# Kernel tuning notes

Hardware: AMD Instinct MI355X
Metric: run time of the kernel (lower is better)

The kernel has to match this reference:

```python
import jax, jax.numpy as jnp
import numpy as np

# J1 Bessel function of the first kind, single-precision rational/asymptotic
# approximation (Numerical Recipes / Abramowitz & Stegun 9.4), matching
# scipy.special.j1 to ~1e-7 relative accuracy. Fully on-device, jit-able.

def bessel_j1(x):
    ax = jnp.abs(x)
    small = ax < 8.0

    # |x| < 8: rational approximation in y = x^2
    y = x * x
    num = x * (72362614232.0 + y * (-7895059235.0 + y * (242396853.1
          + y * (-2972611.439 + y * (15704.48260 + y * (-30.16036606))))))
    den = 144725228442.0 + y * (2300535178.0 + y * (18583304.74
          + y * (99447.43394 + y * (376.9991397 + y))))
    small_val = num / den

    # |x| >= 8: asymptotic expansion; guard ax to avoid div-by-zero in the
    # untaken branch under jnp.where
    ax_s = jnp.where(small, 8.0, ax)
    z = 8.0 / ax_s
    yy = z * z
    xx = ax_s - 2.356194491  # ax - 3*pi/4
    p1 = 1.0 + yy * (0.183105e-2 + yy * (-0.3516396496e-4
         + yy * (0.2457520174e-5 + yy * (-0.240337019e-6))))
    p2 = 0.04687499995 + yy * (-0.2002690873e-3 + yy * (0.8449199096e-5
         + yy * (-0.88228987e-6 + yy * 0.105787412e-6)))
    big_val = jnp.sqrt(0.636619772 / ax_s) * (jnp.cos(xx) * p1
              - z * jnp.sin(xx) * p2) * jnp.sign(x)

    return jnp.where(small, small_val, big_val)


def setup_inputs() -> dict:
    key = jax.random.key(0)
    ks = jax.random.split(key, 7)
    B, D_in, H, D_out = 32768, 64, 2048, 64
    s1 = 1.0 / np.sqrt(D_in)
    s2 = 1.0 / np.sqrt(H)
    return {
        "t": jax.random.normal(ks[0], (B, D_in), dtype=jnp.float32),
        "W1": jax.random.normal(ks[1], (D_in, H), dtype=jnp.float32) * s1,
        "b1": jax.random.normal(ks[2], (H,), dtype=jnp.float32) * s1,
        "W2": jax.random.normal(ks[3], (H, H), dtype=jnp.float32) * s2,
        "b2": jax.random.normal(ks[4], (H,), dtype=jnp.float32) * s2,
        "W3": jax.random.normal(ks[5], (H, D_out), dtype=jnp.float32) * s2,
        "b3": jax.random.normal(ks[6], (D_out,), dtype=jnp.float32) * s2,
    }


def reference(t, W1, b1, W2, b2, W3, b3):
    h = bessel_j1(t @ W1 + b1)        # Linear -> J1 Bessel
    h = jnp.sin(h @ W2 + b2)          # Linear -> sin
    return h @ W3 + b3                # Linear
```

## Files before the change

### kernel.cpp

```cpp
#include <hip/hip_runtime.h>
#include <cstdint>
#include <cstddef>

typedef unsigned short u16;
typedef __attribute__((ext_vector_type(8))) __bf16 bf16x8;
typedef __attribute__((ext_vector_type(4))) float f32x4;


__device__ __forceinline__ u16 f2bf(float f) {
    union { float f; unsigned u; } v; v.f = f;
    unsigned r = v.u + 0x7fffu + ((v.u >> 16) & 1u);
    return (u16)(r >> 16);
}

__device__ __forceinline__ float j1f_approx(float x) {
    float ax = fabsf(x);
    float y = x * x;
    float num = x * (7.2362614232e10f + y * (-7.895059235e9f + y * (2.423968531e8f
              + y * (-2.972611439e6f + y * (1.570448260e4f + y * (-3.016036606e1f))))));
    float den = 1.44725228442e11f + y * (2.300535178e9f + y * (1.858330474e7f
              + y * (9.944743394e4f + y * (3.769991397e2f + y))));
    float r = num / den;
    if (__any(ax >= 8.0f)) {
        float z  = 8.0f / ax;
        float yy = z * z;
        float xx = ax - 2.356194491f;
        float p1 = 1.0f + yy * (0.183105e-2f + yy * (-0.3516396496e-4f
                 + yy * (0.2457520174e-5f + yy * (-0.240337019e-6f))));
        float p2 = 0.04687499995f + yy * (-0.2002690873e-3f + yy * (0.8449199096e-5f
                 + yy * (-0.88228987e-6f + yy * 0.105787412e-6f)));
        float big = sqrtf(0.636619772f / ax) * (__cosf(xx) * p1 - z * __sinf(xx) * p2);
        big = copysignf(big, x);
        if (ax >= 8.0f) r = big;
    }
    return r;
}


__global__ void k_f32_to_bf16(const float* __restrict__ in, u16* __restrict__ out, int n) {
    int i = blockIdx.x * 256 + threadIdx.x;
    if (i < n) out[i] = f2bf(in[i]);
}

__global__ void k_transpose_bf16(const float* __restrict__ in, u16* __restrict__ out,
                                 int K, int N) {
    __shared__ float tile[32][33];
    int n0 = blockIdx.x * 32, k0 = blockIdx.y * 32;
    int tx = threadIdx.x, ty = threadIdx.y;
    #pragma unroll
    for (int i = ty; i < 32; i += 8)
        tile[i][tx] = in[(size_t)(k0 + i) * N + n0 + tx];
    __syncthreads();
    #pragma unroll
    for (int i = ty; i < 32; i += 8)
        out[(size_t)(n0 + i) * K + k0 + tx] = f2bf(tile[tx][i]);
}

__global__ void k_init_out(const float* __restrict__ b3, float* __restrict__ out, int n) {
    int i = blockIdx.x * 256 + threadIdx.x;
    if (i < n) out[i] = b3[i & 63];
}


#define BK 32

template<int BM, int BN, int WTM, int WTN, int EPI>
__global__ __launch_bounds__(256)
void k_gemm_bt(const u16* __restrict__ A, int lda,
               const u16* __restrict__ Bt, int ldb,
               const float* __restrict__ bias,
               void* __restrict__ Cout, int ldc,
               int kstart, int klen)
{
    __shared__ __align__(16) u16 Alds[BM * BK];
    __shared__ __align__(16) u16 Blds[BN * BK];

    const int tid  = threadIdx.x;
    const int lane = tid & 63;
    const int wid  = tid >> 6;
    const int wrow = (wid >> 1) * (WTM * 16);
    const int wcol = (wid & 1) * (WTN * 16);
    const int lr   = lane & 15;
    const int lkb  = (lane >> 4) * 8;

    const int brow = blockIdx.y * BM;
    const int bcol = blockIdx.x * BN;
    const int k0 = kstart + blockIdx.z * klen;
    const int k1 = k0 + klen;

    f32x4 acc[WTM][WTN] = {};

    for (int kk = k0; kk < k1; kk += BK) {
        #pragma unroll
        for (int c = tid; c < BM * 4; c += 256) {
            const u16* g = A + (size_t)(brow + (c >> 2)) * lda + kk + (c & 3) * 8;
            __builtin_amdgcn_global_load_lds(
                (const __attribute__((address_space(1))) void*)g,
                (__attribute__((address_space(3))) void*)(&Alds[c * 8]), 16, 0, 0);
        }
        #pragma unroll
        for (int c = tid; c < BN * 4; c += 256) {
            const u16* g = Bt + (size_t)(bcol + (c >> 2)) * ldb + kk + (c & 3) * 8;
            __builtin_amdgcn_global_load_lds(
                (const __attribute__((address_space(1))) void*)g,
                (__attribute__((address_space(3))) void*)(&Blds[c * 8]), 16, 0, 0);
        }
        __syncthreads();

        bf16x8 af[WTM], bfr[WTN];
        #pragma unroll
        for (int m = 0; m < WTM; ++m)
            af[m] = *(const bf16x8*)&Alds[(wrow + m * 16 + lr) * BK + lkb];
        #pragma unroll
        for (int n = 0; n < WTN; ++n)
            bfr[n] = *(const bf16x8*)&Blds[(wcol + n * 16 + lr) * BK + lkb];
        #pragma unroll
        for (int m = 0; m < WTM; ++m)
            #pragma unroll
            for (int n = 0; n < WTN; ++n)
                acc[m][n] = __builtin_amdgcn_mfma_f32_16x16x32_bf16(
                                af[m], bfr[n], acc[m][n], 0, 0, 0);
        __syncthreads();
    }

    const int rbase = brow + wrow + (lane >> 4) * 4;
    const int cbase = bcol + wcol + lr;
    #pragma unroll
    for (int n = 0; n < WTN; ++n) {
        const int col = cbase + n * 16;
        float bv = 0.0f;
        if constexpr (EPI != 2) bv = bias[col];
        #pragma unroll
        for (int m = 0; m < WTM; ++m) {
            #pragma unroll
            for (int r = 0; r < 4; ++r) {
                const int row = rbase + m * 16 + r;
                float v = acc[m][n][r];
                if constexpr (EPI == 0) {
                    ((u16*)Cout)[(size_t)row * ldc + col] = f2bf(j1f_approx(v + bv));
                } else {
                    atomicAdd(&((float*)Cout)[(size_t)row * ldc + col], v);
                }
            }
        }
    }
}


__global__ __launch_bounds__(512, 2)
void k_gemm256(const u16* __restrict__ A, int lda,
               const u16* __restrict__ Bt, int ldb,
               const float* __restrict__ bias,
               u16* __restrict__ C, int ldc, int K)
{
    __shared__ __align__(16) u16 lds[65536];

    const int tid  = threadIdx.x;
    const int lane = tid & 63;
    const int wid  = tid >> 6;
    const int wr   = wid >> 2;
    const int wc   = wid & 3;
    const int lr   = lane & 15;
    const int kq   = lane >> 4;

    const int nwg  = gridDim.x * gridDim.y;
    const int bid0 = blockIdx.y * gridDim.x + blockIdx.x;
    const int wg   = (bid0 & 7) * (nwg >> 3) + (bid0 >> 3);
    const int bx   = wg % gridDim.x;
    const int by   = wg / gridDim.x;
    const int brow = by * 256;
    const int bcol = bx * 256;

    const int nT = K >> 6;

    auto stage = [&](int tile, int q) {
        const int b = tile & 1, h = q & 1;
        const u16* gb; int ldg; u16* lb;
        if (q < 2) { gb = A  + (size_t)(brow + h * 128) * lda; ldg = lda;
                     lb = &lds[b * 16384 + h * 8192]; }
        else       { gb = Bt + (size_t)(bcol + h * 128) * ldb; ldg = ldb;
                     lb = &lds[32768 + b * 16384 + h * 8192]; }
        #pragma unroll
        for (int r = 0; r < 2; ++r) {
            const int c = r * 512 + tid;
            const int row = c >> 3, slot = c & 7;
            const u16* g = gb + (size_t)row * ldg + tile * 64 + ((slot ^ (row & 7)) << 3);
            __builtin_amdgcn_global_load_lds(
                (const __attribute__((address_space(1))) void*)g,
                (__attribute__((address_space(3))) void*)(lb + c * 8), 16, 0, 0);
        }
    };

    int a_off[8][2], b_off[4][2];
    #pragma unroll
    for (int m = 0; m < 8; ++m) {
        const int row = m * 16 + lr;
        #pragma unroll
        for (int ks = 0; ks < 2; ++ks)
            a_off[m][ks] = row * 64 + ((ks * 32 + kq * 8) ^ ((row & 7) << 3));
    }
    #pragma unroll
    for (int n = 0; n < 4; ++n) {
        const int row = (wc & 1) * 64 + n * 16 + lr;
        #pragma unroll
        for (int ks = 0; ks < 2; ++ks)
            b_off[n][ks] = row * 64 + ((ks * 32 + kq * 8) ^ ((row & 7) << 3));
    }

    f32x4 acc[8][4] = {};
    bf16x8 af[4][2], bf[2][2];

#define RD_A(mh) { _Pragma("unroll") for (int m = 0; m < 4; ++m) \
                   _Pragma("unroll") for (int ks = 0; ks < 2; ++ks) \
                       af[m][ks] = *(const bf16x8*)&la[a_off[(mh)*4 + m][ks]]; }
#define RD_B(nh) { _Pragma("unroll") for (int j = 0; j < 2; ++j) \
                   _Pragma("unroll") for (int ks = 0; ks < 2; ++ks) \
                       bf[j][ks] = *(const bf16x8*)&lb_[b_off[(nh)*2 + j][ks]]; }
#define MMA(mh, nh) { __builtin_amdgcn_s_setprio(1); \
                      _Pragma("unroll") for (int m = 0; m < 4; ++m) \
                      _Pragma("unroll") for (int j = 0; j < 2; ++j) \
                      _Pragma("unroll") for (int ks = 0; ks < 2; ++ks) \
                          acc[(mh)*4 + m][(nh)*2 + j] = \
                              __builtin_amdgcn_mfma_f32_16x16x32_bf16( \
                                  af[m][ks], bf[j][ks], acc[(mh)*4 + m][(nh)*2 + j], 0, 0, 0); \
                      __builtin_amdgcn_s_setprio(0); }
#define BARRIER()  asm volatile("s_barrier" ::: "memory")
#define LGKM0()    asm volatile("s_waitcnt lgkmcnt(0)" ::: "memory")

    stage(0, 0); stage(0, 1); stage(0, 2); stage(0, 3);
    if (nT > 1) {
        stage(1, 0); stage(1, 1);
        asm volatile("s_waitcnt vmcnt(4)" ::: "memory");
    } else {
        asm volatile("s_waitcnt vmcnt(0)" ::: "memory");
    }
    BARRIER();

    for (int t = 0; t < nT; ++t) {
        const int b = t & 1;
        const u16* la  = &lds[b * 16384 + wr * 8192];
        const u16* lb_ = &lds[32768 + b * 16384 + (wc >> 1) * 8192];

        RD_A(0); RD_B(0);
        if (t + 1 < nT) stage(t + 1, 2);
        BARRIER(); LGKM0();
        MMA(0, 0);
        BARRIER();

        RD_B(1);
        if (t + 1 < nT) stage(t + 1, 3);
        BARRIER(); LGKM0();
        MMA(0, 1);
        BARRIER();

        RD_A(1);
        BARRIER(); LGKM0();
        MMA(1, 1);
        BARRIER();

        RD_B(0);
        if (t + 2 < nT) { stage(t + 2, 0); stage(t + 2, 1); }
        BARRIER(); LGKM0();
        MMA(1, 0);
        if (t < nT - 2)       { asm volatile("s_waitcnt vmcnt(4)" ::: "memory"); }
        else if (t == nT - 2) { asm volatile("s_waitcnt vmcnt(0)" ::: "memory"); }
        BARRIER();
    }

#undef RD_A
#undef RD_B
#undef MMA
#undef BARRIER
#undef LGKM0

    #pragma unroll
    for (int n = 0; n < 4; ++n) {
        const int col = bcol + wc * 64 + n * 16 + lr;
        const float bv = bias[col];
        #pragma unroll
        for (int m = 0; m < 8; ++m) {
            const int row = brow + wr * 128 + m * 16 + kq * 4;
            #pragma unroll
            for (int r = 0; r < 4; ++r)
                C[(size_t)(row + r) * ldc + col] = f2bf(__sinf(acc[m][n][r] + bv));
        }
    }
}


extern "C" void kernel_launch(void* const* d_in, const int* in_sizes, int n_in,
                              void* d_out, int out_size, void* d_ws, size_t ws_size,
                              hipStream_t stream) {
    const float* t  = (const float*)d_in[0];
    const float* W1 = (const float*)d_in[1];
    const float* b1 = (const float*)d_in[2];
    const float* W2 = (const float*)d_in[3];
    const float* b2 = (const float*)d_in[4];
    const float* W3 = (const float*)d_in[5];
    const float* b3 = (const float*)d_in[6];
    float* out = (float*)d_out;

    constexpr int B = 32768, Din = 64, H = 2048, Dout = 64;

    char* p = (char*)d_ws;
    u16* t_bf = (u16*)p; p += (size_t)B * Din * 2;
    u16* w1t  = (u16*)p; p += (size_t)H * Din * 2;
    u16* w2t  = (u16*)p; p += (size_t)H * H * 2;
    u16* w3t  = (u16*)p; p += (size_t)Dout * H * 2;
    size_t fixed = (size_t)(p - (char*)d_ws);

    int R = B;
    while (R > 512 && fixed + (size_t)2 * R * H * 2 > ws_size) R >>= 1;
    u16* h1 = (u16*)p;
    u16* h2 = (u16*)(p + (size_t)R * H * 2);

    k_f32_to_bf16<<<(B * Din + 255) / 256, 256, 0, stream>>>(t, t_bf, B * Din);
    k_transpose_bf16<<<dim3(H / 32, Din / 32), dim3(32, 8), 0, stream>>>(W1, w1t, Din, H);
    k_transpose_bf16<<<dim3(H / 32, H / 32), dim3(32, 8), 0, stream>>>(W2, w2t, H, H);
    k_transpose_bf16<<<dim3(Dout / 32, H / 32), dim3(32, 8), 0, stream>>>(W3, w3t, H, Dout);
    k_init_out<<<(out_size + 255) / 256, 256, 0, stream>>>(b3, out, out_size);

    const int SPLITS = 4;
    for (int c0 = 0; c0 < B; c0 += R) {
        const u16* tA = t_bf + (size_t)c0 * Din;
        k_gemm_bt<128, 128, 4, 4, 0><<<dim3(H / 128, R / 128), 256, 0, stream>>>(
            tA, Din, w1t, Din, b1, h1, H, 0, Din);
        k_gemm256<<<dim3(H / 256, R / 256), 512, 0, stream>>>(
            h1, H, w2t, H, b2, h2, H, H);
        k_gemm_bt<128, 64, 4, 2, 2><<<dim3(1, R / 128, SPLITS), 256, 0, stream>>>(
            h2, H, w3t, H, nullptr, out + (size_t)c0 * Dout, Dout, 0, H / SPLITS);
    }
}
```

Before: 410.4 us.

## Restructure big GEMM main loop to overlap LDS fragment reads with MFMA

Reworks the 256x256 GEMM main loop so the B-fragment LDS reads and the second A-fragment read are issued right after the preceding MFMA batch instead of before a barrier plus lgkmcnt(0) wait. Two B fragment register sets are used so the reads can overlap the matrix math, and sched_barrier hints keep the compiler from reordering across phases. Global staging addresses are precomputed once per thread rather than recomputed in a lambda, and the epilogue loads bias values up front. The explicit lgkmcnt waits are removed, which relies on compiler-inserted waits for correctness, and the extra fragment registers raise register pressure.

```diff
diff --git a/kernel.cpp b/kernel.cpp
--- a/kernel.cpp
+++ b/kernel.cpp
@@ -5,6 +5,9 @@
 typedef unsigned short u16;
 typedef __attribute__((ext_vector_type(8))) __bf16 bf16x8;
 typedef __attribute__((ext_vector_type(4))) float f32x4;
+
+#define AS1(p) ((const __attribute__((address_space(1))) void*)(p))
+#define AS3(p) ((__attribute__((address_space(3))) void*)(p))
 
 
 __device__ __forceinline__ u16 f2bf(float f) {
@@ -94,16 +97,12 @@
         #pragma unroll
         for (int c = tid; c < BM * 4; c += 256) {
             const u16* g = A + (size_t)(brow + (c >> 2)) * lda + kk + (c & 3) * 8;
-            __builtin_amdgcn_global_load_lds(
-                (const __attribute__((address_space(1))) void*)g,
-                (__attribute__((address_space(3))) void*)(&Alds[c * 8]), 16, 0, 0);
+            __builtin_amdgcn_global_load_lds(AS1(g), AS3(&Alds[c * 8]), 16, 0, 0);
         }
         #pragma unroll
         for (int c = tid; c < BN * 4; c += 256) {
             const u16* g = Bt + (size_t)(bcol + (c >> 2)) * ldb + kk + (c & 3) * 8;
-            __builtin_amdgcn_global_load_lds(
-                (const __attribute__((address_space(1))) void*)g,
-                (__attribute__((address_space(3))) void*)(&Blds[c * 8]), 16, 0, 0);
+            __builtin_amdgcn_global_load_lds(AS1(g), AS3(&Blds[c * 8]), 16, 0, 0);
         }
         __syncthreads();
 
@@ -173,22 +172,18 @@
 
     const int nT = K >> 6;
 
-    auto stage = [&](int tile, int q) {
-        const int b = tile & 1, h = q & 1;
-        const u16* gb; int ldg; u16* lb;
-        if (q < 2) { gb = A  + (size_t)(brow + h * 128) * lda; ldg = lda;
-                     lb = &lds[b * 16384 + h * 8192]; }
-        else       { gb = Bt + (size_t)(bcol + h * 128) * ldb; ldg = ldb;
-                     lb = &lds[32768 + b * 16384 + h * 8192]; }
-        #pragma unroll
-        for (int r = 0; r < 2; ++r) {
-            const int c = r * 512 + tid;
-            const int row = c >> 3, slot = c & 7;
-            const u16* g = gb + (size_t)row * ldg + tile * 64 + ((slot ^ (row & 7)) << 3);
-            __builtin_amdgcn_global_load_lds(
-                (const __attribute__((address_space(1))) void*)g,
-                (__attribute__((address_space(3))) void*)(lb + c * 8), 16, 0, 0);
-        }
+    const int srow = tid >> 3;
+    const int swz  = (((tid & 7) ^ (srow & 7)) << 3);
+    const u16* pgA0 = A  + (size_t)(brow +       srow) * lda + swz;
+    const u16* pgA1 = A  + (size_t)(brow + 128 + srow) * lda + swz;
+    const u16* pgB0 = Bt + (size_t)(bcol +       srow) * ldb + swz;
+    const u16* pgB1 = Bt + (size_t)(bcol + 128 + srow) * ldb + swz;
+
+    auto stg = [&](const u16* base, int ldg, int tile, u16* l0) {
+        __builtin_amdgcn_global_load_lds(AS1(base + tile * 64),
+                                         AS3(l0 + tid * 8), 16, 0, 0);
+        __builtin_amdgcn_global_load_lds(AS1(base + (size_t)64 * ldg + tile * 64),
+                                         AS3(l0 + 4096 + tid * 8), 16, 0, 0);
     };
 
     int a_off[8][2], b_off[4][2];
@@ -208,28 +203,35 @@
     }
 
     f32x4 acc[8][4] = {};
-    bf16x8 af[4][2], bf[2][2];
+    bf16x8 af[4][2], bf0[2][2], bf1[2][2];
 
 #define RD_A(mh) { _Pragma("unroll") for (int m = 0; m < 4; ++m) \
                    _Pragma("unroll") for (int ks = 0; ks < 2; ++ks) \
                        af[m][ks] = *(const bf16x8*)&la[a_off[(mh)*4 + m][ks]]; }
-#define RD_B(nh) { _Pragma("unroll") for (int j = 0; j < 2; ++j) \
+#define RD_B0()  { _Pragma("unroll") for (int j = 0; j < 2; ++j) \
                    _Pragma("unroll") for (int ks = 0; ks < 2; ++ks) \
-                       bf[j][ks] = *(const bf16x8*)&lb_[b_off[(nh)*2 + j][ks]]; }
-#define MMA(mh, nh) { __builtin_amdgcn_s_setprio(1); \
+                       bf0[j][ks] = *(const bf16x8*)&lb_[b_off[j][ks]]; }
+#define RD_B1()  { _Pragma("unroll") for (int j = 0; j < 2; ++j) \
+                   _Pragma("unroll") for (int ks = 0; ks < 2; ++ks) \
+                       bf1[j][ks] = *(const bf16x8*)&lb_[b_off[2 + j][ks]]; }
+#define MMA(mh, nh, BF) { __builtin_amdgcn_s_setprio(1); \
                       _Pragma("unroll") for (int m = 0; m < 4; ++m) \
                       _Pragma("unroll") for (int j = 0; j < 2; ++j) \
                       _Pragma("unroll") for (int ks = 0; ks < 2; ++ks) \
                           acc[(mh)*4 + m][(nh)*2 + j] = \
                               __builtin_amdgcn_mfma_f32_16x16x32_bf16( \
-                                  af[m][ks], bf[j][ks], acc[(mh)*4 + m][(nh)*2 + j], 0, 0, 0); \
+                                  af[m][ks], BF[j][ks], acc[(mh)*4 + m][(nh)*2 + j], 0, 0, 0); \
                       __builtin_amdgcn_s_setprio(0); }
 #define BARRIER()  asm volatile("s_barrier" ::: "memory")
-#define LGKM0()    asm volatile("s_waitcnt lgkmcnt(0)" ::: "memory")
-
-    stage(0, 0); stage(0, 1); stage(0, 2); stage(0, 3);
+#define SCHED0()   __builtin_amdgcn_sched_barrier(0)
+
+    stg(pgA0, lda, 0, &lds[0]);
+    stg(pgA1, lda, 0, &lds[8192]);
+    stg(pgB0, ldb, 0, &lds[32768]);
+    stg(pgB1, ldb, 0, &lds[32768 + 8192]);
     if (nT > 1) {
-        stage(1, 0); stage(1, 1);
+        stg(pgA0, lda, 1, &lds[16384]);
+        stg(pgA1, lda, 1, &lds[16384 + 8192]);
         asm volatile("s_waitcnt vmcnt(4)" ::: "memory");
     } else {
         asm volatile("s_waitcnt vmcnt(0)" ::: "memory");
@@ -240,49 +242,53 @@
         const int b = t & 1;
         const u16* la  = &lds[b * 16384 + wr * 8192];
         const u16* lb_ = &lds[32768 + b * 16384 + (wc >> 1) * 8192];
-
-        RD_A(0); RD_B(0);
-        if (t + 1 < nT) stage(t + 1, 2);
-        BARRIER(); LGKM0();
-        MMA(0, 0);
+        u16* stA = &lds[b * 16384];
+        u16* stB = &lds[32768 + (b ^ 1) * 16384];
+
+        RD_A(0); RD_B0();
+        if (t + 1 < nT) stg(pgB0, ldb, t + 1, stB);
+        BARRIER(); SCHED0();
+        MMA(0, 0, bf0);
+        RD_B1();
         BARRIER();
 
-        RD_B(1);
-        if (t + 1 < nT) stage(t + 1, 3);
-        BARRIER(); LGKM0();
-        MMA(0, 1);
+        if (t + 1 < nT) stg(pgB1, ldb, t + 1, stB + 8192);
+        BARRIER(); SCHED0();
+        MMA(0, 1, bf1);
+        RD_A(1);
         BARRIER();
 
-        RD_A(1);
-        BARRIER(); LGKM0();
-        MMA(1, 1);
+        SCHED0();
+        MMA(1, 1, bf1);
         BARRIER();
 
-        RD_B(0);
-        if (t + 2 < nT) { stage(t + 2, 0); stage(t + 2, 1); }
-        BARRIER(); LGKM0();
-        MMA(1, 0);
+        if (t + 2 < nT) { stg(pgA0, lda, t + 2, stA); stg(pgA1, lda, t + 2, stA + 8192); }
+        BARRIER(); SCHED0();
+        MMA(1, 0, bf0);
         if (t < nT - 2)       { asm volatile("s_waitcnt vmcnt(4)" ::: "memory"); }
         else if (t == nT - 2) { asm volatile("s_waitcnt vmcnt(0)" ::: "memory"); }
         BARRIER();
     }
 
 #undef RD_A
-#undef RD_B
+#undef RD_B0
+#undef RD_B1
 #undef MMA
 #undef BARRIER
-#undef LGKM0
-
-    #pragma unroll
-    for (int n = 0; n < 4; ++n) {
-        const int col = bcol + wc * 64 + n * 16 + lr;
-        const float bv = bias[col];
-        #pragma unroll
-        for (int m = 0; m < 8; ++m) {
-            const int row = brow + wr * 128 + m * 16 + kq * 4;
+#undef SCHED0
+
+    float bv[4];
+    #pragma unroll
+    for (int n = 0; n < 4; ++n) bv[n] = bias[bcol + wc * 64 + n * 16 + lr];
+    #pragma unroll
+    for (int m = 0; m < 8; ++m) {
+        const int row = brow + wr * 128 + m * 16 + kq * 4;
+        #pragma unroll
+        for (int n = 0; n < 4; ++n) {
+            const int col = bcol + wc * 64 + n * 16 + lr;
             #pragma unroll
             for (int r = 0; r < 4; ++r)
-                C[(size_t)(row + r) * ldc + col] = f2bf(__sinf(acc[m][n][r] + bv));
+                C[(size_t)(row + r) * ldc + col] = f2bf(__sinf(acc[m][n][r] + bv[n]));
         }
     }
 }
```

Measured after the change: 388.2 us. 1.06x faster.
